# Performance work log

Measured on AMD Instinct MI355X. Metric: run time of the kernel, lower is better.

The kernel has to match this reference:

```python
import jax, jax.numpy as jnp
import numpy as np

N = 100000       # nodes
E = 1600000      # edges (avg degree 16)
ND = 64          # node_dim
ED = 1           # edge_dim
HD = 128         # hidden_dim of message MLP


def setup_inputs() -> dict:
    key = jax.random.key(0)
    ks = jax.random.split(key, 12)
    x = jax.random.normal(ks[0], (N, ND), dtype=jnp.float32)
    edge_index = jax.random.randint(ks[1], (2, E), 0, N, dtype=jnp.int32)
    edge_attr = jax.random.normal(ks[2], (E, ED), dtype=jnp.float32)
    # message_net: Linear(2*ND+ED -> HD), ReLU, Linear(HD -> ND); torch default uniform init
    s1 = 1.0 / np.sqrt(2 * ND + ED)
    W1 = jax.random.uniform(ks[3], (HD, 2 * ND + ED), minval=-s1, maxval=s1, dtype=jnp.float32)
    b1 = jax.random.uniform(ks[4], (HD,), minval=-s1, maxval=s1, dtype=jnp.float32)
    s2 = 1.0 / np.sqrt(HD)
    W2 = jax.random.uniform(ks[5], (ND, HD), minval=-s2, maxval=s2, dtype=jnp.float32)
    b2 = jax.random.uniform(ks[6], (ND,), minval=-s2, maxval=s2, dtype=jnp.float32)
    # GRUCell(input=ND, hidden=ND): weight_ih [3*ND, ND], weight_hh [3*ND, ND]
    sg = 1.0 / np.sqrt(ND)
    W_ih = jax.random.uniform(ks[7], (3 * ND, ND), minval=-sg, maxval=sg, dtype=jnp.float32)
    b_ih = jax.random.uniform(ks[8], (3 * ND,), minval=-sg, maxval=sg, dtype=jnp.float32)
    W_hh = jax.random.uniform(ks[9], (3 * ND, ND), minval=-sg, maxval=sg, dtype=jnp.float32)
    b_hh = jax.random.uniform(ks[10], (3 * ND,), minval=-sg, maxval=sg, dtype=jnp.float32)
    return {"x": x, "edge_index": edge_index, "edge_attr": edge_attr,
            "W1": W1, "b1": b1, "W2": W2, "b2": b2,
            "W_ih": W_ih, "b_ih": b_ih, "W_hh": W_hh, "b_hh": b_hh}


def reference(x, edge_index, edge_attr, W1, b1, W2, b2, W_ih, b_ih, W_hh, b_hh):
    src, dst = edge_index[0], edge_index[1]
    # gather + concat + 2-layer MLP message  -> [E, ND]
    m = jnp.concatenate([x[src], x[dst], edge_attr], axis=-1)      # [E, 2*ND+ED]
    m = jax.nn.relu(m @ W1.T + b1) @ W2.T + b2                     # [E, ND]
    # scatter-add aggregate to destination nodes
    aggr = jnp.zeros_like(x).at[dst].add(m)                        # [N, ND]
    # torch GRUCell: input=aggr, hidden=x
    gi = aggr @ W_ih.T + b_ih                                      # [N, 3*ND]
    gh = x @ W_hh.T + b_hh                                         # [N, 3*ND]
    i_r, i_z, i_n = jnp.split(gi, 3, axis=-1)
    h_r, h_z, h_n = jnp.split(gh, 3, axis=-1)
    r = jax.nn.sigmoid(i_r + h_r)
    z = jax.nn.sigmoid(i_z + h_z)
    n = jnp.tanh(i_n + r * h_n)
    return (1.0 - z) * n + z * x
```

## Files before the change

kernel.cpp:

```cpp
#include <hip/hip_runtime.h>

#define NN 100000
#define NE 1600000
#define ND 64
#define HD 128
#define NPB 16
#define NBK (NN / NPB)
#define NPCB 400
#define NCB 250
#define NBA 64
#define CHA (NE / NBA)
#define MSC (NCB * NBA)
#define CSC 16

typedef float f32x4 __attribute__((ext_vector_type(4)));
typedef short s16x8 __attribute__((ext_vector_type(8)));

static __device__ __forceinline__ short f2bf(float f) {
    union { float f; unsigned u; } v; v.f = f;
    unsigned r = (v.u + 0x7fffu + ((v.u >> 16) & 1u)) >> 16;
    return (short)r;
}

#define LSW(n, k)  (((n) << 7) + ((((k) >> 3) ^ ((n) & 15)) << 3) + ((k) & 7))
#define LSW64(n, k) (((n) << 6) + ((((k) >> 3) ^ ((n) & 7)) << 3) + ((k) & 7))

__global__ __launch_bounds__(256) void conv_bf16(const float* __restrict__ x,
                                                 short* __restrict__ xb) {
    const int NG = NN * ND / 8;
    for (int g = blockIdx.x * 256 + threadIdx.x; g < NG; g += gridDim.x * 256) {
        const float4 a = ((const float4*)x)[g * 2];
        const float4 b = ((const float4*)x)[g * 2 + 1];
        s16x8 o;
        o[0] = f2bf(a.x); o[1] = f2bf(a.y); o[2] = f2bf(a.z); o[3] = f2bf(a.w);
        o[4] = f2bf(b.x); o[5] = f2bf(b.y); o[6] = f2bf(b.z); o[7] = f2bf(b.w);
        ((s16x8*)xb)[g] = o;
    }
}

__global__ __launch_bounds__(1024) void histA(const int* __restrict__ ei,
                                              int* __restrict__ gHistA) {
    __shared__ int h[NCB];
    const int tid = threadIdx.x;
    if (tid < NCB) h[tid] = 0;
    __syncthreads();
    const int base = blockIdx.x * CHA;
    for (int i = tid; i < CHA; i += 1024)
        atomicAdd(&h[ei[NE + base + i] / NPCB], 1);
    __syncthreads();
    if (tid < NCB) gHistA[tid * NBA + blockIdx.x] = h[tid];
}

__global__ __launch_bounds__(1024) void scanA(int* __restrict__ g,
                                              int* __restrict__ ticket) {
    __shared__ int A[1024], B[1024];
    const int t  = threadIdx.x;
    const int i0 = t * CSC;
    const int i1 = min(i0 + CSC, MSC);
    int s = 0;
    for (int i = i0; i < i1; ++i) s += g[i];
    A[t] = s;
    __syncthreads();
    int* src = A; int* dst = B;
    for (int off = 1; off < 1024; off <<= 1) {
        int val = src[t];
        if (t >= off) val += src[t - off];
        dst[t] = val;
        __syncthreads();
        int* tmp = src; src = dst; dst = tmp;
    }
    int run = t ? src[t - 1] : 0;
    for (int i = i0; i < i1; ++i) {
        const int v = g[i];
        g[i] = run; run += v;
    }
    if (t == 0) *ticket = 0;
}

__global__ __launch_bounds__(1024) void scatterA(
    const int* __restrict__ ei, const float* __restrict__ ea,
    const int* __restrict__ gBaseA, int2* __restrict__ tsd,
    float* __restrict__ tea) {
    __shared__ int cur[NCB];
    const int tid = threadIdx.x;
    if (tid < NCB) cur[tid] = gBaseA[tid * NBA + blockIdx.x];
    __syncthreads();
    const int base = blockIdx.x * CHA;
    for (int i = tid; i < CHA; i += 1024) {
        const int e = base + i;
        const int sv = ei[e], d = ei[NE + e];
        const float av = ea[e];
        const int pos = atomicAdd(&cur[d / NPCB], 1);
        tsd[pos] = make_int2(sv, d);
        tea[pos] = av;
    }
}

__global__ __launch_bounds__(1024) void scatterB(
    const int2* __restrict__ tsd, const float* __restrict__ tea,
    const int* __restrict__ gBaseA,
    int2* __restrict__ rsd, float* __restrict__ rea,
    int* __restrict__ rowptrB) {
    __shared__ int h[NPCB];
    __shared__ int cur[NPCB];
    __shared__ int A[512], B[512];
    const int c = blockIdx.x;
    const int t = threadIdx.x;
    const int nb0  = c * NPCB;
    const int base = gBaseA[c * NBA];
    const int endc = (c + 1 < NCB) ? gBaseA[(c + 1) * NBA] : NE;

    if (t < NPCB) h[t] = 0;
    __syncthreads();
    for (int i = base + t; i < endc; i += 1024)
        atomicAdd(&h[tsd[i].y - nb0], 1);
    __syncthreads();

    if (t < 512) A[t] = (t < NPCB) ? h[t] : 0;
    __syncthreads();
    int* src = A; int* dst = B;
    for (int off = 1; off < 512; off <<= 1) {
        if (t < 512) {
            int val = src[t];
            if (t >= off) val += src[t - off];
            dst[t] = val;
        }
        __syncthreads();
        int* tmp = src; src = dst; dst = tmp;
    }
    if (t < NPCB) {
        const int excl = t ? src[t - 1] : 0;
        cur[t] = base + excl;
        if ((t & (NPB - 1)) == 0)
            rowptrB[(nb0 + t) >> 4] = base + excl;
    }
    if (c == NCB - 1 && t == 0) rowptrB[NBK] = NE;
    __syncthreads();

    for (int i = base + t; i < endc; i += 1024) {
        const int2 sd = tsd[i];
        const float av = tea[i];
        const int pos = atomicAdd(&cur[sd.y - nb0], 1);
        rsd[pos] = sd;
        rea[pos] = av;
    }
}

__global__ __launch_bounds__(512) void msg_mfma3(
    const short* __restrict__ xb, const int2* __restrict__ rsd,
    const float* __restrict__ rea, const int* __restrict__ rowptrB,
    int* __restrict__ ticket,
    const float* __restrict__ W1, const float* __restrict__ b1,
    const float* __restrict__ W2, const float* __restrict__ b2,
    float* __restrict__ aggr)
{
    __shared__ short w1lds[128 * 128];
    __shared__ short w2lds[64 * 128];
    __shared__ short vbuf[8 * 16 * 128];
    __shared__ float albuf[8 * NPB * 64];

    const int tid = threadIdx.x;
    for (int i = tid; i < 128 * 128; i += 512) {
        int n = i >> 7, k = i & 127;
        w1lds[LSW(n, k)] = f2bf(W1[n * 129 + k]);
    }
    for (int i = tid; i < 64 * 128; i += 512) {
        int n = i >> 7, k = i & 127;
        w2lds[LSW(n, k)] = f2bf(W2[n * 128 + k]);
    }
    __syncthreads();

    const int lane = tid & 63;
    const int w    = tid >> 6;
    const int nlo  = lane & 15;
    const int q    = lane >> 4;

    float w1l[8], b1v[8], b2v[4];
    #pragma unroll
    for (int t = 0; t < 8; ++t) {
        w1l[t] = W1[(nlo + 16 * t) * 129 + 128];
        b1v[t] = b1[nlo + 16 * t];
    }
    #pragma unroll
    for (int t = 0; t < 4; ++t) b2v[t] = b2[nlo + 16 * t];

    short* myv = vbuf + w * (16 * 128);
    float* vf  = (float*)myv;
    float* al  = albuf + w * (NPB * 64);

    for (;;) {
        int bk = 0;
        if (lane == 0) bk = atomicAdd(ticket, 1);
        bk = __shfl(bk, 0, 64);
        if (bk >= NBK) break;

        const int n0    = bk * NPB;
        const int start = rowptrB[bk];
        const int end   = rowptrB[bk + 1];

        const f32x4 z = {0.f, 0.f, 0.f, 0.f};
        #pragma unroll
        for (int j = 0; j < 4; ++j) ((f32x4*)al)[lane + 64 * j] = z;

        if (start < end) {
            int  idx0 = min(start + nlo, end - 1);
            int2 sd   = rsd[idx0];
            float eav = rea[idx0];
            s16x8 a0 = *(const s16x8*)(xb + sd.x * ND + (q << 3));
            s16x8 a1 = *(const s16x8*)(xb + sd.x * ND + 32 + (q << 3));
            s16x8 a2 = *(const s16x8*)(xb + sd.y * ND + (q << 3));
            s16x8 a3 = *(const s16x8*)(xb + sd.y * ND + 32 + (q << 3));

            for (int p = start; p < end; p += 16) {
                const int dv = sd.y;

                const int  idxn = min(p + 16 + nlo, end - 1);
                const int2 sdn  = rsd[idxn];
                const float ean = rea[idxn];

                f32x4 acc[8];
                #pragma unroll
                for (int t = 0; t < 8; ++t) { acc[t][0] = b1v[t]; acc[t][1] = b1v[t]; acc[t][2] = b1v[t]; acc[t][3] = b1v[t]; }

                __builtin_amdgcn_s_setprio(1);
                #pragma unroll
                for (int kk = 0; kk < 4; ++kk) {
                    const s16x8 af = (kk == 0) ? a0 : (kk == 1) ? a1 : (kk == 2) ? a2 : a3;
                    const int chunk = ((kk * 4 + q) ^ nlo) << 3;
                    #pragma unroll
                    for (int t = 0; t < 8; ++t) {
                        const s16x8 bf = *(const s16x8*)(w1lds + ((nlo + 16 * t) << 7) + chunk);
                        acc[t] = __builtin_amdgcn_mfma_f32_16x16x32_bf16(af, bf, acc[t], 0, 0, 0);
                    }
                }
                __builtin_amdgcn_s_setprio(0);

                const s16x8 n0_ = *(const s16x8*)(xb + sdn.x * ND + (q << 3));
                const s16x8 n1_ = *(const s16x8*)(xb + sdn.x * ND + 32 + (q << 3));
                const s16x8 n2_ = *(const s16x8*)(xb + sdn.y * ND + (q << 3));
                const s16x8 n3_ = *(const s16x8*)(xb + sdn.y * ND + 32 + (q << 3));

                float ear[4];
                #pragma unroll
                for (int r = 0; r < 4; ++r) ear[r] = __shfl(eav, q * 4 + r, 64);
                #pragma unroll
                for (int t = 0; t < 8; ++t) {
                    #pragma unroll
                    for (int r = 0; r < 4; ++r) {
                        const float hv = fmaxf(acc[t][r] + ear[r] * w1l[t], 0.f);
                        const int m = q * 4 + r;
                        const int k = nlo + 16 * t;
                        myv[LSW(m, k)] = f2bf(hv);
                    }
                }

                f32x4 acc2[4];
                #pragma unroll
                for (int t = 0; t < 4; ++t) { acc2[t][0] = b2v[t]; acc2[t][1] = b2v[t]; acc2[t][2] = b2v[t]; acc2[t][3] = b2v[t]; }

                __builtin_amdgcn_s_setprio(1);
                #pragma unroll
                for (int kk = 0; kk < 4; ++kk) {
                    const int chunk = ((kk * 4 + q) ^ nlo) << 3;
                    const s16x8 af = *(const s16x8*)(myv + (nlo << 7) + chunk);
                    #pragma unroll
                    for (int t = 0; t < 4; ++t) {
                        const s16x8 bf = *(const s16x8*)(w2lds + ((nlo + 16 * t) << 7) + chunk);
                        acc2[t] = __builtin_amdgcn_mfma_f32_16x16x32_bf16(af, bf, acc2[t], 0, 0, 0);
                    }
                }
                __builtin_amdgcn_s_setprio(0);

                #pragma unroll
                for (int t = 0; t < 4; ++t) {
                    #pragma unroll
                    for (int r = 0; r < 4; ++r) {
                        const int m = q * 4 + r;
                        vf[m * 64 + ((nlo + 16 * t) ^ (q << 3))] = acc2[t][r];
                    }
                }

                const int nrows = min(16, end - p);
                float vals[16];
                #pragma unroll
                for (int r = 0; r < 16; ++r)
                    vals[r] = vf[r * 64 + (lane ^ ((r >> 2) << 3))];

                int   prev = __builtin_amdgcn_readlane(dv, 0);
                float sum  = vals[0];
                #pragma unroll
                for (int r = 1; r < 16; ++r) {
                    if (r < nrows) {
                        const int dd = __builtin_amdgcn_readlane(dv, r);
                        if (dd == prev) sum += vals[r];
                        else {
                            al[(prev - n0) * 64 + lane] += sum;
                            prev = dd; sum = vals[r];
                        }
                    }
                }
                al[(prev - n0) * 64 + lane] += sum;

                sd = sdn; eav = ean;
                a0 = n0_; a1 = n1_; a2 = n2_; a3 = n3_;
            }
        }

        f32x4* dstv = (f32x4*)(aggr + n0 * 64);
        #pragma unroll
        for (int j = 0; j < 4; ++j)
            dstv[lane + 64 * j] = ((f32x4*)al)[lane + 64 * j];
    }
}

__global__ __launch_bounds__(512) void gru_mfma(
    const float* __restrict__ x, const float* __restrict__ aggr,
    const float* __restrict__ Wih, const float* __restrict__ bih,
    const float* __restrict__ Whh, const float* __restrict__ bhh,
    float* __restrict__ out)
{
    __shared__ short wi[192 * 64];
    __shared__ short wh[192 * 64];

    const int tid = threadIdx.x;
    for (int i = tid; i < 192 * 64; i += 512) {
        int n = i >> 6, k = i & 63;
        wi[LSW64(n, k)] = f2bf(Wih[n * 64 + k]);
        wh[LSW64(n, k)] = f2bf(Whh[n * 64 + k]);
    }
    __syncthreads();

    const int lane = tid & 63;
    const int w    = tid >> 6;
    const int nlo  = lane & 15;
    const int q    = lane >> 4;

    float bi[12], bh[12];
    #pragma unroll
    for (int t = 0; t < 12; ++t) { bi[t] = bih[16 * t + nlo]; bh[t] = bhh[16 * t + nlo]; }

    const int gw = blockIdx.x * 8 + w;
    const int nw = gridDim.x * 8;

    for (int tile = gw; tile < NN / 16; tile += nw) {
        const int n0 = tile * 16;
        f32x4 ai[12], ah[12];
        #pragma unroll
        for (int t = 0; t < 12; ++t) {
            ai[t][0] = bi[t]; ai[t][1] = bi[t]; ai[t][2] = bi[t]; ai[t][3] = bi[t];
            ah[t][0] = bh[t]; ah[t][1] = bh[t]; ah[t][2] = bh[t]; ah[t][3] = bh[t];
        }

        #pragma unroll
        for (int kk = 0; kk < 2; ++kk) {
            const int coff = (n0 + nlo) * ND + kk * 32 + q * 8;
            const float4 a0 = *(const float4*)(aggr + coff);
            const float4 a1 = *(const float4*)(aggr + coff + 4);
            const float4 x0 = *(const float4*)(x + coff);
            const float4 x1 = *(const float4*)(x + coff + 4);
            s16x8 fA, fX;
            fA[0] = f2bf(a0.x); fA[1] = f2bf(a0.y); fA[2] = f2bf(a0.z); fA[3] = f2bf(a0.w);
            fA[4] = f2bf(a1.x); fA[5] = f2bf(a1.y); fA[6] = f2bf(a1.z); fA[7] = f2bf(a1.w);
            fX[0] = f2bf(x0.x); fX[1] = f2bf(x0.y); fX[2] = f2bf(x0.z); fX[3] = f2bf(x0.w);
            fX[4] = f2bf(x1.x); fX[5] = f2bf(x1.y); fX[6] = f2bf(x1.z); fX[7] = f2bf(x1.w);
            const int chunk = kk * 4 + q;
            #pragma unroll
            for (int t = 0; t < 12; ++t) {
                const int rb = 16 * t + nlo;
                const int boff = (rb << 6) + (((chunk) ^ (rb & 7)) << 3);
                const s16x8 bI = *(const s16x8*)(wi + boff);
                const s16x8 bH = *(const s16x8*)(wh + boff);
                ai[t] = __builtin_amdgcn_mfma_f32_16x16x32_bf16(fA, bI, ai[t], 0, 0, 0);
                ah[t] = __builtin_amdgcn_mfma_f32_16x16x32_bf16(fX, bH, ah[t], 0, 0, 0);
            }
        }

        #pragma unroll
        for (int t = 0; t < 4; ++t) {
            #pragma unroll
            for (int r = 0; r < 4; ++r) {
                const int node = n0 + q * 4 + r;
                const int c    = nlo + 16 * t;
                const float rr = 1.f / (1.f + __expf(-(ai[t][r] + ah[t][r])));
                const float zz = 1.f / (1.f + __expf(-(ai[t + 4][r] + ah[t + 4][r])));
                const float nv = ai[t + 8][r] + rr * ah[t + 8][r];
                const float nn = 2.f / (1.f + __expf(-2.f * nv)) - 1.f;
                const float xv = x[node * ND + c];
                out[node * ND + c] = (1.f - zz) * nn + zz * xv;
            }
        }
    }
}

extern "C" void kernel_launch(void* const* d_in, const int* in_sizes, int n_in,
                              void* d_out, int out_size, void* d_ws, size_t ws_size,
                              hipStream_t stream) {
    const float* x   = (const float*)d_in[0];
    const int*   ei  = (const int*)d_in[1];
    const float* ea  = (const float*)d_in[2];
    const float* W1  = (const float*)d_in[3];
    const float* b1  = (const float*)d_in[4];
    const float* W2  = (const float*)d_in[5];
    const float* b2  = (const float*)d_in[6];
    const float* Wih = (const float*)d_in[7];
    const float* bih = (const float*)d_in[8];
    const float* Whh = (const float*)d_in[9];
    const float* bhh = (const float*)d_in[10];
    float* out = (float*)d_out;

    char* ws = (char*)d_ws;
    float* aggr    = (float*)(ws);
    int2*  tsd     = (int2*) (ws);
    float* tea     = (float*)(ws + 12800000);
    short* xb      = (short*)(ws + 25600000);
    int2*  rsd     = (int2*) (ws + 38400000);
    float* rea     = (float*)(ws + 51200000);
    int*   gHistA  = (int*)  (ws + 57600000);
    int*   rowptrB = (int*)  (ws + 57664000);
    int*   ticket  = (int*)  (ws + 57689004);

    hipLaunchKernelGGL(conv_bf16, dim3(512), dim3(256), 0, stream, x, xb);
    hipLaunchKernelGGL(histA, dim3(NBA), dim3(1024), 0, stream, ei, gHistA);
    hipLaunchKernelGGL(scanA, dim3(1), dim3(1024), 0, stream, gHistA, ticket);
    hipLaunchKernelGGL(scatterA, dim3(NBA), dim3(1024), 0, stream,
                       ei, ea, gHistA, tsd, tea);
    hipLaunchKernelGGL(scatterB, dim3(NCB), dim3(1024), 0, stream,
                       tsd, tea, gHistA, rsd, rea, rowptrB);
    hipLaunchKernelGGL(msg_mfma3, dim3(512), dim3(512), 0, stream,
                       xb, rsd, rea, rowptrB, ticket, W1, b1, W2, b2, aggr);
    hipLaunchKernelGGL(gru_mfma, dim3(256), dim3(512), 0, stream,
                       x, aggr, Wih, bih, Whh, bhh, out);
}
```

Measured before the change: 518.4 us.

## Pack edge records, fuse bf16 conversion into histogram, shrink node blocks, deepen prefetch

Edge records are packed into a single int2 holding the source index, the local destination offset and the edge attribute as raw bits. This removes the separate edge-attribute arrays and cuts scatter traffic. The bf16 conversion of x is folded into the histogram kernel, which saves one launch. Node blocks per work ticket drop from 16 to 8, the edge index prefetch goes two iterations ahead with the x-row gathers issued before the MFMA work, and grid sizes for the message and GRU kernels change. Smaller blocks mean more ticket atomics and edge groups with partial occupancy, and the packing assumes node indices fit in 17 bits.

Result: slower. 529.1 us (+2.0%).

```diff
diff --git a/kernel.cpp b/kernel.cpp
--- a/kernel.cpp
+++ b/kernel.cpp
@@ -4,10 +4,11 @@
 #define NE 1600000
 #define ND 64
 #define HD 128
-#define NPB 16
+#define NPB 8
 #define NBK (NN / NPB)
 #define NPCB 400
 #define NCB 250
+#define NFPC (NPCB / NPB)
 #define NBA 64
 #define CHA (NE / NBA)
 #define MSC (NCB * NBA)
@@ -16,6 +17,7 @@
 typedef float f32x4 __attribute__((ext_vector_type(4)));
 typedef short s16x8 __attribute__((ext_vector_type(8)));
 
+
 static __device__ __forceinline__ short f2bf(float f) {
     union { float f; unsigned u; } v; v.f = f;
     unsigned r = (v.u + 0x7fffu + ((v.u >> 16) & 1u)) >> 16;
@@ -25,10 +27,22 @@
 #define LSW(n, k)  (((n) << 7) + ((((k) >> 3) ^ ((n) & 15)) << 3) + ((k) & 7))
 #define LSW64(n, k) (((n) << 6) + ((((k) >> 3) ^ ((n) & 7)) << 3) + ((k) & 7))
 
-__global__ __launch_bounds__(256) void conv_bf16(const float* __restrict__ x,
-                                                 short* __restrict__ xb) {
+__global__ __launch_bounds__(1024) void histA(const int* __restrict__ ei,
+                                              int* __restrict__ gHistA,
+                                              const float* __restrict__ x,
+                                              short* __restrict__ xb) {
+    __shared__ int h[NCB];
+    const int tid = threadIdx.x;
+    if (tid < NCB) h[tid] = 0;
+    __syncthreads();
+    const int base = blockIdx.x * CHA;
+    for (int i = tid; i < CHA; i += 1024)
+        atomicAdd(&h[ei[NE + base + i] / NPCB], 1);
+    __syncthreads();
+    if (tid < NCB) gHistA[tid * NBA + blockIdx.x] = h[tid];
+
     const int NG = NN * ND / 8;
-    for (int g = blockIdx.x * 256 + threadIdx.x; g < NG; g += gridDim.x * 256) {
+    for (int g = blockIdx.x * 1024 + tid; g < NG; g += NBA * 1024) {
         const float4 a = ((const float4*)x)[g * 2];
         const float4 b = ((const float4*)x)[g * 2 + 1];
         s16x8 o;
@@ -36,19 +50,6 @@
         o[4] = f2bf(b.x); o[5] = f2bf(b.y); o[6] = f2bf(b.z); o[7] = f2bf(b.w);
         ((s16x8*)xb)[g] = o;
     }
-}
-
-__global__ __launch_bounds__(1024) void histA(const int* __restrict__ ei,
-                                              int* __restrict__ gHistA) {
-    __shared__ int h[NCB];
-    const int tid = threadIdx.x;
-    if (tid < NCB) h[tid] = 0;
-    __syncthreads();
-    const int base = blockIdx.x * CHA;
-    for (int i = tid; i < CHA; i += 1024)
-        atomicAdd(&h[ei[NE + base + i] / NPCB], 1);
-    __syncthreads();
-    if (tid < NCB) gHistA[tid * NBA + blockIdx.x] = h[tid];
 }
 
 __global__ __launch_bounds__(1024) void scanA(int* __restrict__ g,
@@ -79,8 +80,7 @@
 
 __global__ __launch_bounds__(1024) void scatterA(
     const int* __restrict__ ei, const float* __restrict__ ea,
-    const int* __restrict__ gBaseA, int2* __restrict__ tsd,
-    float* __restrict__ tea) {
+    const int* __restrict__ gBaseA, int2* __restrict__ tsd) {
     __shared__ int cur[NCB];
     const int tid = threadIdx.x;
     if (tid < NCB) cur[tid] = gBaseA[tid * NBA + blockIdx.x];
@@ -90,17 +90,16 @@
         const int e = base + i;
         const int sv = ei[e], d = ei[NE + e];
         const float av = ea[e];
-        const int pos = atomicAdd(&cur[d / NPCB], 1);
-        tsd[pos] = make_int2(sv, d);
-        tea[pos] = av;
+        const int c = d / NPCB;
+        const int dloc = d - c * NPCB;
+        const int pos = atomicAdd(&cur[c], 1);
+        tsd[pos] = make_int2(sv | (dloc << 17), __float_as_int(av));
     }
 }
 
 __global__ __launch_bounds__(1024) void scatterB(
-    const int2* __restrict__ tsd, const float* __restrict__ tea,
-    const int* __restrict__ gBaseA,
-    int2* __restrict__ rsd, float* __restrict__ rea,
-    int* __restrict__ rowptrB) {
+    const int2* __restrict__ tsd, const int* __restrict__ gBaseA,
+    int2* __restrict__ rsd, int* __restrict__ rowptrB) {
     __shared__ int h[NPCB];
     __shared__ int cur[NPCB];
     __shared__ int A[512], B[512];
@@ -113,7 +112,7 @@
     if (t < NPCB) h[t] = 0;
     __syncthreads();
     for (int i = base + t; i < endc; i += 1024)
-        atomicAdd(&h[tsd[i].y - nb0], 1);
+        atomicAdd(&h[(tsd[i].x >> 17) & 0x1FF], 1);
     __syncthreads();
 
     if (t < 512) A[t] = (t < NPCB) ? h[t] : 0;
@@ -132,24 +131,21 @@
         const int excl = t ? src[t - 1] : 0;
         cur[t] = base + excl;
         if ((t & (NPB - 1)) == 0)
-            rowptrB[(nb0 + t) >> 4] = base + excl;
+            rowptrB[(nb0 + t) / NPB] = base + excl;
     }
     if (c == NCB - 1 && t == 0) rowptrB[NBK] = NE;
     __syncthreads();
 
     for (int i = base + t; i < endc; i += 1024) {
-        const int2 sd = tsd[i];
-        const float av = tea[i];
-        const int pos = atomicAdd(&cur[sd.y - nb0], 1);
-        rsd[pos] = sd;
-        rea[pos] = av;
+        const int2 r = tsd[i];
+        const int pos = atomicAdd(&cur[(r.x >> 17) & 0x1FF], 1);
+        rsd[pos] = r;
     }
 }
 
 __global__ __launch_bounds__(512) void msg_mfma3(
     const short* __restrict__ xb, const int2* __restrict__ rsd,
-    const float* __restrict__ rea, const int* __restrict__ rowptrB,
-    int* __restrict__ ticket,
+    const int* __restrict__ rowptrB, int* __restrict__ ticket,
     const float* __restrict__ W1, const float* __restrict__ b1,
     const float* __restrict__ W2, const float* __restrict__ b2,
     float* __restrict__ aggr)
@@ -195,28 +191,36 @@
         if (bk >= NBK) break;
 
         const int n0    = bk * NPB;
+        const int cbase = (bk / NFPC) * NPCB;
+        const int bdl   = (bk % NFPC) * NPB;
         const int start = rowptrB[bk];
         const int end   = rowptrB[bk + 1];
 
         const f32x4 z = {0.f, 0.f, 0.f, 0.f};
         #pragma unroll
-        for (int j = 0; j < 4; ++j) ((f32x4*)al)[lane + 64 * j] = z;
+        for (int j = 0; j < 2; ++j) ((f32x4*)al)[lane + 64 * j] = z;
 
         if (start < end) {
-            int  idx0 = min(start + nlo, end - 1);
-            int2 sd   = rsd[idx0];
-            float eav = rea[idx0];
-            s16x8 a0 = *(const s16x8*)(xb + sd.x * ND + (q << 3));
-            s16x8 a1 = *(const s16x8*)(xb + sd.x * ND + 32 + (q << 3));
-            s16x8 a2 = *(const s16x8*)(xb + sd.y * ND + (q << 3));
-            s16x8 a3 = *(const s16x8*)(xb + sd.y * ND + 32 + (q << 3));
+            int2 e0 = rsd[min(start + nlo, end - 1)];
+            int2 e1 = rsd[min(start + 16 + nlo, end - 1)];
+            const int sr0 = (e0.x & 0x1FFFF) * ND + (q << 3);
+            const int dr0 = (cbase + ((e0.x >> 17) & 0x1FF)) * ND + (q << 3);
+            s16x8 a0 = *(const s16x8*)(xb + sr0);
+            s16x8 a1 = *(const s16x8*)(xb + sr0 + 32);
+            s16x8 a2 = *(const s16x8*)(xb + dr0);
+            s16x8 a3 = *(const s16x8*)(xb + dr0 + 32);
 
             for (int p = start; p < end; p += 16) {
-                const int dv = sd.y;
-
-                const int  idxn = min(p + 16 + nlo, end - 1);
-                const int2 sdn  = rsd[idxn];
-                const float ean = rea[idxn];
+                const int2 e2 = rsd[min(p + 32 + nlo, end - 1)];
+                const int sr1 = (e1.x & 0x1FFFF) * ND + (q << 3);
+                const int dr1 = (cbase + ((e1.x >> 17) & 0x1FF)) * ND + (q << 3);
+                const s16x8 n0_ = *(const s16x8*)(xb + sr1);
+                const s16x8 n1_ = *(const s16x8*)(xb + sr1 + 32);
+                const s16x8 n2_ = *(const s16x8*)(xb + dr1);
+                const s16x8 n3_ = *(const s16x8*)(xb + dr1 + 32);
+
+                const int   dlv = (e0.x >> 17) & 0x1FF;
+                const float eav = __int_as_float(e0.y);
 
                 f32x4 acc[8];
                 #pragma unroll
@@ -235,11 +239,6 @@
                 }
                 __builtin_amdgcn_s_setprio(0);
 
-                const s16x8 n0_ = *(const s16x8*)(xb + sdn.x * ND + (q << 3));
-                const s16x8 n1_ = *(const s16x8*)(xb + sdn.x * ND + 32 + (q << 3));
-                const s16x8 n2_ = *(const s16x8*)(xb + sdn.y * ND + (q << 3));
-                const s16x8 n3_ = *(const s16x8*)(xb + sdn.y * ND + 32 + (q << 3));
-
                 float ear[4];
                 #pragma unroll
                 for (int r = 0; r < 4; ++r) ear[r] = __shfl(eav, q * 4 + r, 64);
@@ -286,29 +285,29 @@
                 for (int r = 0; r < 16; ++r)
                     vals[r] = vf[r * 64 + (lane ^ ((r >> 2) << 3))];
 
-                int   prev = __builtin_amdgcn_readlane(dv, 0);
+                int   prev = __builtin_amdgcn_readlane(dlv, 0);
                 float sum  = vals[0];
                 #pragma unroll
                 for (int r = 1; r < 16; ++r) {
                     if (r < nrows) {
-                        const int dd = __builtin_amdgcn_readlane(dv, r);
+                        const int dd = __builtin_amdgcn_readlane(dlv, r);
                         if (dd == prev) sum += vals[r];
                         else {
-                            al[(prev - n0) * 64 + lane] += sum;
+                            al[(prev - bdl) * 64 + lane] += sum;
                             prev = dd; sum = vals[r];
                         }
                     }
                 }
-                al[(prev - n0) * 64 + lane] += sum;
-
-                sd = sdn; eav = ean;
+                al[(prev - bdl) * 64 + lane] += sum;
+
+                e0 = e1; e1 = e2;
                 a0 = n0_; a1 = n1_; a2 = n2_; a3 = n3_;
             }
         }
 
         f32x4* dstv = (f32x4*)(aggr + n0 * 64);
         #pragma unroll
-        for (int j = 0; j < 4; ++j)
+        for (int j = 0; j < 2; ++j)
             dstv[lane + 64 * j] = ((f32x4*)al)[lane + 64 * j];
     }
 }
@@ -411,23 +410,20 @@
     char* ws = (char*)d_ws;
     float* aggr    = (float*)(ws);
     int2*  tsd     = (int2*) (ws);
-    float* tea     = (float*)(ws + 12800000);
     short* xb      = (short*)(ws + 25600000);
     int2*  rsd     = (int2*) (ws + 38400000);
-    float* rea     = (float*)(ws + 51200000);
-    int*   gHistA  = (int*)  (ws + 57600000);
-    int*   rowptrB = (int*)  (ws + 57664000);
-    int*   ticket  = (int*)  (ws + 57689004);
-
-    hipLaunchKernelGGL(conv_bf16, dim3(512), dim3(256), 0, stream, x, xb);
-    hipLaunchKernelGGL(histA, dim3(NBA), dim3(1024), 0, stream, ei, gHistA);
+    int*   gHistA  = (int*)  (ws + 51200000);
+    int*   rowptrB = (int*)  (ws + 51264000);
+    int*   ticket  = (int*)  (ws + 51314004);
+
+    hipLaunchKernelGGL(histA, dim3(NBA), dim3(1024), 0, stream, ei, gHistA, x, xb);
     hipLaunchKernelGGL(scanA, dim3(1), dim3(1024), 0, stream, gHistA, ticket);
     hipLaunchKernelGGL(scatterA, dim3(NBA), dim3(1024), 0, stream,
-                       ei, ea, gHistA, tsd, tea);
+                       ei, ea, gHistA, tsd);
     hipLaunchKernelGGL(scatterB, dim3(NCB), dim3(1024), 0, stream,
-                       tsd, tea, gHistA, rsd, rea, rowptrB);
-    hipLaunchKernelGGL(msg_mfma3, dim3(512), dim3(512), 0, stream,
-                       xb, rsd, rea, rowptrB, ticket, W1, b1, W2, b2, aggr);
-    hipLaunchKernelGGL(gru_mfma, dim3(256), dim3(512), 0, stream,
+                       tsd, gHistA, rsd, rowptrB);
+    hipLaunchKernelGGL(msg_mfma3, dim3(256), dim3(512), 0, stream,
+                       xb, rsd, rowptrB, ticket, W1, b1, W2, b2, aggr);
+    hipLaunchKernelGGL(gru_mfma, dim3(512), dim3(512), 0, stream,
                        x, aggr, Wih, bih, Whh, bhh, out);
 }
```
